# Kernel optimization log

Hardware: AMD Instinct MI355X
Metric: run time of the kernel (lower is better)

The kernel has to match this reference:

```python
import jax, jax.numpy as jnp
import numpy as np

HIDDEN = 768
N_HEADS = 12
D_HEAD = 64
B, T = 4, 2048


def setup_inputs() -> dict:
    key = jax.random.key(0)
    ks = jax.random.split(key, 5)
    s = 0.02
    return {
        "x": jax.random.normal(ks[0], (B, T, HIDDEN), dtype=jnp.float32),
        "w_q": jax.random.normal(ks[1], (HIDDEN, HIDDEN), dtype=jnp.float32) * s,
        "w_k": jax.random.normal(ks[2], (HIDDEN, HIDDEN), dtype=jnp.float32) * s,
        "w_v": jax.random.normal(ks[3], (HIDDEN, HIDDEN), dtype=jnp.float32) * s,
        "w_o": jax.random.normal(ks[4], (HIDDEN, HIDDEN), dtype=jnp.float32) * s,
    }


def reference(x, w_q, w_k, w_v, w_o):
    # nn.Linear applies x @ W^T; weights here are [out, in] like torch.
    b, t, h = x.shape
    q = (x @ w_q.T).reshape(b, t, N_HEADS, D_HEAD)
    k = (x @ w_k.T).reshape(b, t, N_HEADS, D_HEAD)
    v = (x @ w_v.T).reshape(b, t, N_HEADS, D_HEAD)
    # scores: [b, heads, t, t]
    scores = jnp.einsum("bqhd,bkhd->bhqk", q, k) / jnp.sqrt(jnp.float32(D_HEAD))
    weights = jax.nn.softmax(scores, axis=-1)
    # dropout p=0.0 -> identity
    ctx = jnp.einsum("bhqk,bkhd->bqhd", weights, v).reshape(b, t, h)
    return ctx @ w_o.T
```

## Files before the change

### kernel.cpp

```cpp
#include <hip/hip_runtime.h>

#define HIDDEN 768
#define NH 12
#define DH 64
#define BB 4
#define TT 2048
#define MTOT (BB * TT)

typedef __bf16 bf16x8 __attribute__((ext_vector_type(8)));
typedef short s16x8 __attribute__((ext_vector_type(8)));
typedef float f32x4 __attribute__((ext_vector_type(4)));

__device__ __forceinline__ unsigned short f2b(float f) {
    unsigned u = __builtin_bit_cast(unsigned, f);
    u += 0x7fffu + ((u >> 16) & 1u);
    return (unsigned short)(u >> 16);
}

typedef const __attribute__((address_space(1))) unsigned int* gas_ptr;
typedef __attribute__((address_space(3))) unsigned int* las_ptr;
__device__ __forceinline__ void gload16(const void* g, void* l) {
    __builtin_amdgcn_global_load_lds((gas_ptr)(uintptr_t)g, (las_ptr)(uintptr_t)l, 16, 0, 0);
}

__global__ __launch_bounds__(256) void cvt_all(const float* __restrict__ x,
                                               const float* __restrict__ wq,
                                               const float* __restrict__ wk,
                                               const float* __restrict__ wv,
                                               const float* __restrict__ wo,
                                               unsigned short* __restrict__ out) {
    const size_t NX8 = (size_t)MTOT * HIDDEN / 8;
    const size_t NW8 = (size_t)HIDDEN * HIDDEN / 8;
    size_t i = (size_t)blockIdx.x * 256 + threadIdx.x;
    const float* src;
    size_t off = i;
    float scale = 1.0f;
    if (i < NX8) { src = x; }
    else if (i < NX8 + NW8) { src = wq; off = i - NX8; scale = 0.18033688011112042f; }
    else if (i < NX8 + 2 * NW8) { src = wk; off = i - NX8 - NW8; }
    else if (i < NX8 + 3 * NW8) { src = wv; off = i - NX8 - 2 * NW8; }
    else { src = wo; off = i - NX8 - 3 * NW8; }
    const float4* p = (const float4*)src + off * 2;
    float4 a = p[0], b = p[1];
    union { uint4 u; unsigned short s[8]; } t;
    t.s[0] = f2b(a.x * scale); t.s[1] = f2b(a.y * scale);
    t.s[2] = f2b(a.z * scale); t.s[3] = f2b(a.w * scale);
    t.s[4] = f2b(b.x * scale); t.s[5] = f2b(b.y * scale);
    t.s[6] = f2b(b.z * scale); t.s[7] = f2b(b.w * scale);
    ((uint4*)out)[i] = t.u;
}

template <int OUTF>
__device__ __forceinline__ void gemm_body(const unsigned short* __restrict__ A,
                                          const unsigned short* __restrict__ Bm,
                                          float* __restrict__ Cf,
                                          unsigned short* __restrict__ Cb,
                                          int mBase, int nBase, int N) {
    __shared__ __align__(16) unsigned short Al[2][128][64];
    __shared__ __align__(16) unsigned short Bl[2][128][64];
    const int tid = threadIdx.x;
    const int lane = tid & 63;
    const int wave = tid >> 6;
    const int quad = lane >> 4;
    const int l16 = lane & 15;
    const int mw = (wave >> 1) * 64;
    const int nw = (wave & 1) * 64;
    const int srow = wave * 32 + (lane >> 3);
    const int swiz = ((lane & 7) ^ (lane >> 3)) * 8;
    const unsigned short* Asrc = A + (size_t)(mBase + srow) * HIDDEN + swiz;
    const unsigned short* Bsrc = Bm + (size_t)(nBase + srow) * HIDDEN + swiz;

    f32x4 acc[4][4];
#pragma unroll
    for (int mt = 0; mt < 4; ++mt)
#pragma unroll
        for (int nt = 0; nt < 4; ++nt) acc[mt][nt] = (f32x4){0.f, 0.f, 0.f, 0.f};

    auto stage = [&](int buf, int kb) {
#pragma unroll
        for (int i = 0; i < 4; ++i) {
            gload16(Asrc + (size_t)i * 8 * HIDDEN + kb * 64, &Al[buf][wave * 32 + i * 8][0]);
            gload16(Bsrc + (size_t)i * 8 * HIDDEN + kb * 64, &Bl[buf][wave * 32 + i * 8][0]);
        }
    };

    stage(0, 0);
    for (int kb = 0; kb < HIDDEN / 64; ++kb) {
        __syncthreads();
        if (kb + 1 < HIDDEN / 64) stage((kb + 1) & 1, kb + 1);
        const int buf = kb & 1;
#pragma unroll
        for (int ks = 0; ks < 2; ++ks) {
            const int cc = ((ks * 4 + quad) ^ (l16 & 7)) * 8;
            bf16x8 af[4], bf[4];
#pragma unroll
            for (int t = 0; t < 4; ++t) {
                af[t] = *(const bf16x8*)&Al[buf][mw + t * 16 + l16][cc];
                bf[t] = *(const bf16x8*)&Bl[buf][nw + t * 16 + l16][cc];
            }
#pragma unroll
            for (int mt = 0; mt < 4; ++mt)
#pragma unroll
                for (int nt = 0; nt < 4; ++nt)
                    acc[mt][nt] = __builtin_amdgcn_mfma_f32_16x16x32_bf16(
                        af[mt], bf[nt], acc[mt][nt], 0, 0, 0);
        }
    }

#pragma unroll
    for (int mt = 0; mt < 4; ++mt)
#pragma unroll
        for (int nt = 0; nt < 4; ++nt)
#pragma unroll
            for (int r = 0; r < 4; ++r) {
                int row = mBase + mw + mt * 16 + quad * 4 + r;
                int col = nBase + nw + nt * 16 + l16;
                float v = acc[mt][nt][r];
                if (OUTF)
                    Cf[(size_t)row * N + col] = v;
                else
                    Cb[(size_t)row * N + col] = f2b(v);
            }
}

__global__ __launch_bounds__(256) void gemm_qkv(const unsigned short* __restrict__ A,
                                                const unsigned short* __restrict__ W0,
                                                unsigned short* __restrict__ C0) {
    const int wsel = blockIdx.x / 6;
    const int nb = blockIdx.x % 6;
    gemm_body<0>(A, W0 + (size_t)wsel * HIDDEN * HIDDEN, nullptr,
                 C0 + (size_t)wsel * MTOT * HIDDEN, blockIdx.y * 128, nb * 128, HIDDEN);
}

__global__ __launch_bounds__(256) void gemm_out(const unsigned short* __restrict__ A,
                                                const unsigned short* __restrict__ Bm,
                                                float* __restrict__ Cf) {
    gemm_body<1>(A, Bm, Cf, nullptr, blockIdx.y * 128, blockIdx.x * 128, HIDDEN);
}

__global__ __launch_bounds__(256) void vt_kernel(const unsigned short* __restrict__ in,
                                                 unsigned short* __restrict__ out) {
    __shared__ unsigned short T[64][73];
    const int tid = threadIdx.x;
    const int r0 = blockIdx.x * 64;
    const int c0 = blockIdx.y * 64;
#pragma unroll
    for (int p = 0; p < 2; ++p) {
        int idx = p * 256 + tid;
        int r = idx >> 3, c = idx & 7;
        union { uint4 u; unsigned short s[8]; } t;
        t.u = *(const uint4*)&in[(size_t)(r0 + r) * HIDDEN + c0 + c * 8];
#pragma unroll
        for (int e = 0; e < 8; ++e) T[r][c * 8 + e] = t.s[e];
    }
    __syncthreads();
#pragma unroll
    for (int p = 0; p < 2; ++p) {
        int idx = p * 256 + tid;
        int cc = idx >> 3, rc = idx & 7;
        union { uint4 u; unsigned short s[8]; } t;
#pragma unroll
        for (int e = 0; e < 8; ++e) t.s[e] = T[rc * 8 + e][cc];
        *(uint4*)&out[(size_t)(c0 + cc) * MTOT + r0 + rc * 8] = t.u;
    }
}

__global__ __launch_bounds__(256) void attn_kernel(const unsigned short* __restrict__ Qg,
                                                   const unsigned short* __restrict__ Kg,
                                                   const unsigned short* __restrict__ VTg,
                                                   unsigned short* __restrict__ Ctx) {
    __shared__ __align__(16) unsigned short Kl[2][64][64];
    __shared__ __align__(16) unsigned short Vl[2][64][64];
    __shared__ __align__(16) unsigned short Pl[4][32][68];
    const int tid = threadIdx.x;
    const int lane = tid & 63;
    const int wave = tid >> 6;
    const int quad = lane >> 4;
    const int l16 = lane & 15;
    const int qt = blockIdx.x;
    const int bh = blockIdx.y;
    const int b = bh / NH, h = bh % NH;
    const int qrow0 = b * TT + qt * 128;
    const int col0 = h * DH;

    const int srow = wave * 16 + (lane >> 3);
    const int swiz = ((lane & 7) ^ (lane >> 3)) * 8;
    const unsigned short* Ksrc = Kg + (size_t)(b * TT + srow) * HIDDEN + col0 + swiz;
    const unsigned short* Vsrc = VTg + (size_t)(col0 + srow) * MTOT + b * TT + swiz;

    auto stage = [&](int buf, int kt) {
#pragma unroll
        for (int i = 0; i < 2; ++i) {
            gload16(Ksrc + (size_t)(kt * 64 + i * 8) * HIDDEN, &Kl[buf][wave * 16 + i * 8][0]);
            gload16(Vsrc + (size_t)(i * 8) * MTOT + kt * 64, &Vl[buf][wave * 16 + i * 8][0]);
        }
    };

    bf16x8 qf[2][2];
#pragma unroll
    for (int mt = 0; mt < 2; ++mt)
#pragma unroll
        for (int ks = 0; ks < 2; ++ks)
            qf[mt][ks] = *(const bf16x8*)&Qg[(size_t)(qrow0 + wave * 32 + mt * 16 + l16) * HIDDEN +
                                             col0 + ks * 32 + quad * 8];

    s16x8 osv;
#pragma unroll
    for (int e = 0; e < 8; ++e) osv[e] = 0x3F80;
    const bf16x8 ones = __builtin_bit_cast(bf16x8, osv);

    f32x4 o[2][4];
    f32x4 lacc[2];
#pragma unroll
    for (int mt = 0; mt < 2; ++mt) {
        lacc[mt] = (f32x4){0.f, 0.f, 0.f, 0.f};
#pragma unroll
        for (int nt = 0; nt < 4; ++nt) o[mt][nt] = (f32x4){0.f, 0.f, 0.f, 0.f};
    }

    stage(0, 0);
    for (int kt = 0; kt < TT / 64; ++kt) {
        __syncthreads();
        if (kt + 1 < TT / 64) stage((kt + 1) & 1, kt + 1);
        const int buf = kt & 1;

        f32x4 s[2][4];
#pragma unroll
        for (int mt = 0; mt < 2; ++mt)
#pragma unroll
            for (int nt = 0; nt < 4; ++nt) s[mt][nt] = (f32x4){0.f, 0.f, 0.f, 0.f};
#pragma unroll
        for (int ks = 0; ks < 2; ++ks) {
            const int cc = ((ks * 4 + quad) ^ (l16 & 7)) * 8;
            bf16x8 kf[4];
#pragma unroll
            for (int nt = 0; nt < 4; ++nt)
                kf[nt] = *(const bf16x8*)&Kl[buf][nt * 16 + l16][cc];
#pragma unroll
            for (int mt = 0; mt < 2; ++mt)
#pragma unroll
                for (int nt = 0; nt < 4; ++nt)
                    s[mt][nt] = __builtin_amdgcn_mfma_f32_16x16x32_bf16(qf[mt][ks], kf[nt],
                                                                        s[mt][nt], 0, 0, 0);
        }

#pragma unroll
        for (int mt = 0; mt < 2; ++mt) {
            int row0 = mt * 16 + quad * 4;
#pragma unroll
            for (int nt = 0; nt < 4; ++nt) {
                int col = nt * 16 + l16;
#pragma unroll
                for (int r = 0; r < 4; ++r) {
                    float pv = __builtin_amdgcn_exp2f(s[mt][nt][r]);
                    Pl[wave][row0 + r][col] =
                        (unsigned short)(__builtin_bit_cast(unsigned, pv) >> 16);
                }
            }
        }

#pragma unroll
        for (int ks = 0; ks < 2; ++ks) {
            const int cc = ((ks * 4 + quad) ^ (l16 & 7)) * 8;
            bf16x8 pf[2], vf[4];
#pragma unroll
            for (int mt = 0; mt < 2; ++mt)
                pf[mt] = *(const bf16x8*)&Pl[wave][mt * 16 + l16][ks * 32 + quad * 8];
#pragma unroll
            for (int nt = 0; nt < 4; ++nt)
                vf[nt] = *(const bf16x8*)&Vl[buf][nt * 16 + l16][cc];
#pragma unroll
            for (int mt = 0; mt < 2; ++mt)
                lacc[mt] = __builtin_amdgcn_mfma_f32_16x16x32_bf16(pf[mt], ones, lacc[mt], 0, 0, 0);
#pragma unroll
            for (int mt = 0; mt < 2; ++mt)
#pragma unroll
                for (int nt = 0; nt < 4; ++nt)
                    o[mt][nt] = __builtin_amdgcn_mfma_f32_16x16x32_bf16(pf[mt], vf[nt],
                                                                        o[mt][nt], 0, 0, 0);
        }
    }

#pragma unroll
    for (int mt = 0; mt < 2; ++mt)
#pragma unroll
        for (int r = 0; r < 4; ++r) {
            float inv = __builtin_amdgcn_rcpf(lacc[mt][r]);
            int row = qrow0 + wave * 32 + mt * 16 + quad * 4 + r;
#pragma unroll
            for (int nt = 0; nt < 4; ++nt)
                Ctx[(size_t)row * HIDDEN + col0 + nt * 16 + l16] = f2b(o[mt][nt][r] * inv);
        }
}

extern "C" void kernel_launch(void* const* d_in, const int* in_sizes, int n_in,
                              void* d_out, int out_size, void* d_ws, size_t ws_size,
                              hipStream_t stream) {
    const float* x = (const float*)d_in[0];
    const float* wq = (const float*)d_in[1];
    const float* wk = (const float*)d_in[2];
    const float* wv = (const float*)d_in[3];
    const float* wo = (const float*)d_in[4];
    float* out = (float*)d_out;

    const size_t NX = (size_t)MTOT * HIDDEN;
    const size_t NW = (size_t)HIDDEN * HIDDEN;
    unsigned short* ws = (unsigned short*)d_ws;
    unsigned short* xb = ws;
    unsigned short* wqb = xb + NX;
    unsigned short* wob = wqb + 3 * NW;
    unsigned short* qb = wob + NW;
    unsigned short* kb = qb + NX;
    unsigned short* vb = kb + NX;
    unsigned short* vtb = vb + NX;
    unsigned short* cb = vb;

    cvt_all<<<(int)((NX + 4 * NW) / 8 / 256), 256, 0, stream>>>(x, wq, wk, wv, wo, xb);

    gemm_qkv<<<dim3(18, MTOT / 128), 256, 0, stream>>>(xb, wqb, qb);

    vt_kernel<<<dim3(MTOT / 64, HIDDEN / 64), 256, 0, stream>>>(vb, vtb);

    attn_kernel<<<dim3(TT / 128, BB * NH), 256, 0, stream>>>(qb, kb, vtb, cb);

    gemm_out<<<dim3(6, MTOT / 128), 256, 0, stream>>>(cb, wob, out);
}
```

Measured before the change: 229.7 us.

## Fuse V transpose into QKV GEMM epilogue and pack P stores

The V projection blocks of the QKV GEMM now write their output directly in transposed layout, so the standalone transpose kernel and its extra global round-trip are removed. In attention, the QK^T MFMA operands are swapped so each lane holds consecutive key columns. Lanes then pack pairs of bf16 probabilities and store 8 bytes to LDS at a time instead of scalar 16-bit stores. The transposed epilogue uses narrower, strided global stores, which may coalesce less well than the old row-major writes.

Result: faster. 222.3 us (-3.2%).

```diff
diff --git a/kernel.cpp b/kernel.cpp
--- a/kernel.cpp
+++ b/kernel.cpp
@@ -15,6 +15,11 @@
     unsigned u = __builtin_bit_cast(unsigned, f);
     u += 0x7fffu + ((u >> 16) & 1u);
     return (unsigned short)(u >> 16);
+}
+
+__device__ __forceinline__ unsigned pack_bf16(float a, float b) {
+    return __builtin_amdgcn_perm(__builtin_bit_cast(unsigned, b),
+                                 __builtin_bit_cast(unsigned, a), 0x07060302u);
 }
 
 typedef const __attribute__((address_space(1))) unsigned int* gas_ptr;
@@ -50,7 +55,7 @@
     ((uint4*)out)[i] = t.u;
 }
 
-template <int OUTF>
+template <int MODE>
 __device__ __forceinline__ void gemm_body(const unsigned short* __restrict__ A,
                                           const unsigned short* __restrict__ Bm,
                                           float* __restrict__ Cf,
@@ -110,59 +115,47 @@
 #pragma unroll
     for (int mt = 0; mt < 4; ++mt)
 #pragma unroll
-        for (int nt = 0; nt < 4; ++nt)
-#pragma unroll
-            for (int r = 0; r < 4; ++r) {
-                int row = mBase + mw + mt * 16 + quad * 4 + r;
+        for (int nt = 0; nt < 4; ++nt) {
+            if (MODE == 2) {
+                ushort4 h;
+                h.x = f2b(acc[mt][nt][0]); h.y = f2b(acc[mt][nt][1]);
+                h.z = f2b(acc[mt][nt][2]); h.w = f2b(acc[mt][nt][3]);
+                int m0 = mBase + mw + mt * 16 + quad * 4;
                 int col = nBase + nw + nt * 16 + l16;
-                float v = acc[mt][nt][r];
-                if (OUTF)
-                    Cf[(size_t)row * N + col] = v;
-                else
-                    Cb[(size_t)row * N + col] = f2b(v);
+                *(ushort4*)&Cb[(size_t)col * MTOT + m0] = h;
+            } else {
+#pragma unroll
+                for (int r = 0; r < 4; ++r) {
+                    int row = mBase + mw + mt * 16 + quad * 4 + r;
+                    int col = nBase + nw + nt * 16 + l16;
+                    float v = acc[mt][nt][r];
+                    if (MODE == 1)
+                        Cf[(size_t)row * N + col] = v;
+                    else
+                        Cb[(size_t)row * N + col] = f2b(v);
+                }
             }
+        }
 }
 
 __global__ __launch_bounds__(256) void gemm_qkv(const unsigned short* __restrict__ A,
                                                 const unsigned short* __restrict__ W0,
-                                                unsigned short* __restrict__ C0) {
+                                                unsigned short* __restrict__ C0,
+                                                unsigned short* __restrict__ VT) {
     const int wsel = blockIdx.x / 6;
     const int nb = blockIdx.x % 6;
-    gemm_body<0>(A, W0 + (size_t)wsel * HIDDEN * HIDDEN, nullptr,
-                 C0 + (size_t)wsel * MTOT * HIDDEN, blockIdx.y * 128, nb * 128, HIDDEN);
+    if (wsel < 2)
+        gemm_body<0>(A, W0 + (size_t)wsel * HIDDEN * HIDDEN, nullptr,
+                     C0 + (size_t)wsel * MTOT * HIDDEN, blockIdx.y * 128, nb * 128, HIDDEN);
+    else
+        gemm_body<2>(A, W0 + 2 * (size_t)HIDDEN * HIDDEN, nullptr, VT,
+                     blockIdx.y * 128, nb * 128, HIDDEN);
 }
 
 __global__ __launch_bounds__(256) void gemm_out(const unsigned short* __restrict__ A,
                                                 const unsigned short* __restrict__ Bm,
                                                 float* __restrict__ Cf) {
     gemm_body<1>(A, Bm, Cf, nullptr, blockIdx.y * 128, blockIdx.x * 128, HIDDEN);
-}
-
-__global__ __launch_bounds__(256) void vt_kernel(const unsigned short* __restrict__ in,
-                                                 unsigned short* __restrict__ out) {
-    __shared__ unsigned short T[64][73];
-    const int tid = threadIdx.x;
-    const int r0 = blockIdx.x * 64;
-    const int c0 = blockIdx.y * 64;
-#pragma unroll
-    for (int p = 0; p < 2; ++p) {
-        int idx = p * 256 + tid;
-        int r = idx >> 3, c = idx & 7;
-        union { uint4 u; unsigned short s[8]; } t;
-        t.u = *(const uint4*)&in[(size_t)(r0 + r) * HIDDEN + c0 + c * 8];
-#pragma unroll
-        for (int e = 0; e < 8; ++e) T[r][c * 8 + e] = t.s[e];
-    }
-    __syncthreads();
-#pragma unroll
-    for (int p = 0; p < 2; ++p) {
-        int idx = p * 256 + tid;
-        int cc = idx >> 3, rc = idx & 7;
-        union { uint4 u; unsigned short s[8]; } t;
-#pragma unroll
-        for (int e = 0; e < 8; ++e) t.s[e] = T[rc * 8 + e][cc];
-        *(uint4*)&out[(size_t)(c0 + cc) * MTOT + r0 + rc * 8] = t.u;
-    }
 }
 
 __global__ __launch_bounds__(256) void attn_kernel(const unsigned short* __restrict__ Qg,
@@ -171,7 +164,7 @@
                                                    unsigned short* __restrict__ Ctx) {
     __shared__ __align__(16) unsigned short Kl[2][64][64];
     __shared__ __align__(16) unsigned short Vl[2][64][64];
-    __shared__ __align__(16) unsigned short Pl[4][32][68];
+    __shared__ __align__(16) unsigned int Pl[4][32][36];
     const int tid = threadIdx.x;
     const int lane = tid & 63;
     const int wave = tid >> 6;
@@ -240,22 +233,23 @@
             for (int mt = 0; mt < 2; ++mt)
 #pragma unroll
                 for (int nt = 0; nt < 4; ++nt)
-                    s[mt][nt] = __builtin_amdgcn_mfma_f32_16x16x32_bf16(qf[mt][ks], kf[nt],
+                    s[mt][nt] = __builtin_amdgcn_mfma_f32_16x16x32_bf16(kf[nt], qf[mt][ks],
                                                                         s[mt][nt], 0, 0, 0);
         }
 
 #pragma unroll
         for (int mt = 0; mt < 2; ++mt) {
-            int row0 = mt * 16 + quad * 4;
+            const int row = mt * 16 + l16;
 #pragma unroll
             for (int nt = 0; nt < 4; ++nt) {
-                int col = nt * 16 + l16;
-#pragma unroll
-                for (int r = 0; r < 4; ++r) {
-                    float pv = __builtin_amdgcn_exp2f(s[mt][nt][r]);
-                    Pl[wave][row0 + r][col] =
-                        (unsigned short)(__builtin_bit_cast(unsigned, pv) >> 16);
-                }
+                float p0 = __builtin_amdgcn_exp2f(s[mt][nt][0]);
+                float p1 = __builtin_amdgcn_exp2f(s[mt][nt][1]);
+                float p2 = __builtin_amdgcn_exp2f(s[mt][nt][2]);
+                float p3 = __builtin_amdgcn_exp2f(s[mt][nt][3]);
+                uint2 w;
+                w.x = pack_bf16(p0, p1);
+                w.y = pack_bf16(p2, p3);
+                *(uint2*)&Pl[wave][row][nt * 8 + quad * 2] = w;
             }
         }
 
@@ -265,7 +259,8 @@
             bf16x8 pf[2], vf[4];
 #pragma unroll
             for (int mt = 0; mt < 2; ++mt)
-                pf[mt] = *(const bf16x8*)&Pl[wave][mt * 16 + l16][ks * 32 + quad * 8];
+                pf[mt] = *(const bf16x8*)((const unsigned short*)&Pl[wave][mt * 16 + l16][0] +
+                                          ks * 32 + quad * 8);
 #pragma unroll
             for (int nt = 0; nt < 4; ++nt)
                 vf[nt] = *(const bf16x8*)&Vl[buf][nt * 16 + l16][cc];
@@ -311,15 +306,12 @@
     unsigned short* wob = wqb + 3 * NW;
     unsigned short* qb = wob + NW;
     unsigned short* kb = qb + NX;
-    unsigned short* vb = kb + NX;
-    unsigned short* vtb = vb + NX;
-    unsigned short* cb = vb;
+    unsigned short* cb = kb + NX;
+    unsigned short* vtb = cb + NX;
 
     cvt_all<<<(int)((NX + 4 * NW) / 8 / 256), 256, 0, stream>>>(x, wq, wk, wv, wo, xb);
 
-    gemm_qkv<<<dim3(18, MTOT / 128), 256, 0, stream>>>(xb, wqb, qb);
-
-    vt_kernel<<<dim3(MTOT / 64, HIDDEN / 64), 256, 0, stream>>>(vb, vtb);
+    gemm_qkv<<<dim3(18, MTOT / 128), 256, 0, stream>>>(xb, wqb, qb, vtb);
 
     attn_kernel<<<dim3(TT / 128, BB * NH), 256, 0, stream>>>(qb, kb, vtb, cb);
 
```
